# Kernel optimization log

Measured on AMD Instinct MI355X. Metric: run time of the kernel, lower is better.

Reference implementation:

```python
import jax, jax.numpy as jnp
import numpy as np

D_MODEL = 1024
D_STATE = 16
D_CONV = 4
EXPAND = 2
D_INNER = D_MODEL * EXPAND
LN_EPS = 1e-5


def setup_inputs() -> dict:
    key = jax.random.key(0)
    ks = jax.random.split(key, 12)
    s = lambda fan_in: 1.0 / np.sqrt(fan_in)
    return {
        "x": jax.random.normal(ks[0], (4, 2048, D_MODEL), dtype=jnp.float32),
        "ln_w": jnp.ones((D_MODEL,), jnp.float32),
        "ln_b": jnp.zeros((D_MODEL,), jnp.float32),
        "W_in": jax.random.uniform(ks[1], (D_MODEL, 2 * D_INNER), jnp.float32, -s(D_MODEL), s(D_MODEL)),
        "b_in": jax.random.uniform(ks[2], (2 * D_INNER,), jnp.float32, -s(D_MODEL), s(D_MODEL)),
        "conv_w": jax.random.uniform(ks[3], (D_INNER, 1, D_CONV), jnp.float32, -s(D_CONV), s(D_CONV)),
        "conv_b": jax.random.uniform(ks[4], (D_INNER,), jnp.float32, -s(D_CONV), s(D_CONV)),
        "A_log": jax.random.normal(ks[5], (D_INNER, D_STATE), jnp.float32),
        "D": jax.random.normal(ks[6], (D_INNER,), jnp.float32),
        "W_x": jax.random.uniform(ks[7], (D_INNER, 2 * D_STATE), jnp.float32, -s(D_INNER), s(D_INNER)),
        "b_x": jax.random.uniform(ks[8], (2 * D_STATE,), jnp.float32, -s(D_INNER), s(D_INNER)),
        "W_out": jax.random.uniform(ks[9], (D_INNER, D_MODEL), jnp.float32, -s(D_INNER), s(D_INNER)),
        "b_out": jax.random.uniform(ks[10], (D_MODEL,), jnp.float32, -s(D_INNER), s(D_INNER)),
    }


def _selective_scan(xc, deltaA, Bm, Cm):
    # xc: (b, s, di), deltaA: (di, n), Bm/Cm: (b, s, n)
    b, _, di = xc.shape
    n = Bm.shape[-1]
    h0 = jnp.zeros((b, di, n), xc.dtype)

    def step(h, inp):
        xt, bt, ct = inp  # (b,di), (b,n), (b,n)
        h = deltaA[None] * h + xt[:, :, None] * bt[:, None, :]
        y = jnp.einsum('bin,bn->bi', h, ct)
        return h, y

    xs = (jnp.swapaxes(xc, 0, 1), jnp.swapaxes(Bm, 0, 1), jnp.swapaxes(Cm, 0, 1))
    _, ys = jax.lax.scan(step, h0, xs)  # ys: (s, b, di)
    return jnp.swapaxes(ys, 0, 1)


def reference(x, ln_w, ln_b, W_in, b_in, conv_w, conv_b, A_log, D, W_x, b_x, W_out, b_out):
    residual = x
    mu = jnp.mean(x, -1, keepdims=True)
    var = jnp.mean((x - mu) ** 2, -1, keepdims=True)
    xn = (x - mu) * jax.lax.rsqrt(var + LN_EPS) * ln_w + ln_b
    xg = xn @ W_in + b_in
    x_main, gate = jnp.split(xg, 2, axis=-1)  # (b,s,di) each
    # causal depthwise conv1d (left pad d_conv-1 == torch pad both + slice [:s])
    xt = jnp.swapaxes(x_main, 1, 2)  # (b, di, s)
    xc = jax.lax.conv_general_dilated(
        xt, conv_w, window_strides=(1,), padding=[(D_CONV - 1, 0)],
        feature_group_count=D_INNER, dimension_numbers=('NCH', 'OIH', 'NCH'))
    xc = xc + conv_b[None, :, None]
    x_conv = jax.nn.silu(jnp.swapaxes(xc, 1, 2))  # (b,s,di)
    ssm = x_conv @ W_x + b_x
    Bm, Cm = jnp.split(ssm, 2, axis=-1)  # (b,s,n)
    deltaA = jnp.exp(-jnp.exp(A_log))  # exp(A), A = -exp(A_log)
    y = _selective_scan(x_conv, deltaA, Bm, Cm)
    y = y + x_conv * D[None, None, :]
    y = y * jax.nn.silu(gate)
    out = y @ W_out + b_out
    return out + residual
```

## Files before the change

kernel.cpp:

```cpp
#include <hip/hip_runtime.h>
#include <stdint.h>

typedef unsigned short u16;
typedef short bf16x8 __attribute__((ext_vector_type(8)));
typedef float f32x4 __attribute__((ext_vector_type(4)));

#define TOKENS 8192
#define SEQ 2048
#define DM 1024
#define DI 2048
#define NCH 32
#define CLEN 64

__device__ __forceinline__ float bf2f(u16 u) {
  union { uint32_t i; float f; } v; v.i = ((uint32_t)u) << 16; return v.f;
}
__device__ __forceinline__ u16 f2bf(float f) {
  union { float f; uint32_t i; } v; v.f = f;
  uint32_t r = v.i + 0x7FFFu + ((v.i >> 16) & 1u);
  return (u16)(r >> 16);
}

__device__ __forceinline__ void g2lds16(const void* g, void* l) {
  __builtin_amdgcn_global_load_lds(
      (const __attribute__((address_space(1))) uint32_t*)g,
      (__attribute__((address_space(3))) uint32_t*)l, 16, 0, 0);
}

__global__ __launch_bounds__(256)
void transpose_to_bf16(const float* __restrict__ src, u16* __restrict__ dst,
                       int R, int C) {
  __shared__ float tile[64][65];
  const int i = threadIdx.x;
  const int tilesC = C >> 6;
  const int br = blockIdx.x / tilesC, bc = blockIdx.x % tilesC;
  const int r0 = br << 6, c0 = bc << 6;
  const int cx = (i & 15) << 2, ry = i >> 4;
#pragma unroll
  for (int p = 0; p < 4; ++p) {
    int row = ry + p * 16;
    float4 v = *(const float4*)&src[(size_t)(r0 + row) * C + c0 + cx];
    tile[row][cx + 0] = v.x; tile[row][cx + 1] = v.y;
    tile[row][cx + 2] = v.z; tile[row][cx + 3] = v.w;
  }
  __syncthreads();
#pragma unroll
  for (int p = 0; p < 4; ++p) {
    int cr = ry + p * 16;
    ushort4 o;
    o.x = f2bf(tile[cx + 0][cr]); o.y = f2bf(tile[cx + 1][cr]);
    o.z = f2bf(tile[cx + 2][cr]); o.w = f2bf(tile[cx + 3][cr]);
    *(ushort4*)&dst[(size_t)(c0 + cr) * R + r0 + cx] = o;
  }
}

__global__ __launch_bounds__(256)
void txpose_wx(const float* __restrict__ src, u16* __restrict__ dst) {
  const int gid = blockIdx.x * 256 + threadIdx.x;
  const int k = gid >> 5, n = gid & 31;
  dst[(size_t)n * DI + k] = f2bf(src[gid]);
}

__global__ __launch_bounds__(256)
void layernorm_bf16(const float* __restrict__ x, const float* __restrict__ lw,
                    const float* __restrict__ lb, u16* __restrict__ xn) {
  const int row = blockIdx.x, tid = threadIdx.x;
  const float4 v = *(const float4*)&x[(size_t)row * DM + tid * 4];
  float s = v.x + v.y + v.z + v.w;
  float q = v.x * v.x + v.y * v.y + v.z * v.z + v.w * v.w;
#pragma unroll
  for (int m = 1; m < 64; m <<= 1) { s += __shfl_xor(s, m); q += __shfl_xor(q, m); }
  __shared__ float red[8];
  const int w = tid >> 6, lane = tid & 63;
  if (lane == 0) { red[w] = s; red[4 + w] = q; }
  __syncthreads();
  s = red[0] + red[1] + red[2] + red[3];
  q = red[4] + red[5] + red[6] + red[7];
  const float mu = s * (1.f / DM);
  const float var = q * (1.f / DM) - mu * mu;
  const float rs = rsqrtf(var + 1e-5f);
  const float4 wv = *(const float4*)&lw[tid * 4];
  const float4 bv = *(const float4*)&lb[tid * 4];
  ushort4 o;
  o.x = f2bf((v.x - mu) * rs * wv.x + bv.x);
  o.y = f2bf((v.y - mu) * rs * wv.y + bv.y);
  o.z = f2bf((v.z - mu) * rs * wv.z + bv.z);
  o.w = f2bf((v.w - mu) * rs * wv.w + bv.w);
  *(ushort4*)&xn[(size_t)row * DM + tid * 4] = o;
}

#define TILE256 (2 * 256 * 64)
__global__ __launch_bounds__(512, 2)
void gemm8(const u16* __restrict__ A, const u16* __restrict__ Bt,
           const float* __restrict__ bias, u16* __restrict__ out,
           int M, int N, int K) {
  __shared__ __align__(16) u16 lds[2 * TILE256];
  const int tid = threadIdx.x, wid = tid >> 6, lane = tid & 63;
  const int ntiles = N >> 8;
  int bid = blockIdx.x;
  {
    const int cpx = gridDim.x >> 3;
    bid = (bid & 7) * cpx + (bid >> 3);
  }
  const int tm = bid / ntiles, tn = bid % ntiles;
  const int m0 = tm << 8, n0 = tn << 8;
  const int wm = (wid >> 2) * 128, wn = (wid & 3) * 64;
  const int fr = lane & 15, fg = lane >> 4;
  const int c0 = (fg ^ (fr & 7)) << 4;
  const int NK = K >> 6;

  f32x4 acc[8][4];
#pragma unroll
  for (int mi = 0; mi < 8; ++mi)
#pragma unroll
    for (int ni = 0; ni < 4; ++ni) acc[mi][ni] = (f32x4){0.f, 0.f, 0.f, 0.f};

  auto stage_unit = [&](int T, int isB, int u) {
    const int kt = T << 6;
    const int row = u * 64 + (tid >> 3);
    const int l = (tid & 7) ^ (row & 7);
    const u16* src = (isB ? Bt + (size_t)(n0 + row) * K
                          : A + (size_t)(m0 + row) * K) + kt + l * 8;
    g2lds16(src, lds + (size_t)(T & 1) * TILE256 + isB * 16384 + u * 4096 + tid * 8);
  };

#pragma unroll
  for (int u = 0; u < 4; ++u) stage_unit(0, 1, u);
#pragma unroll
  for (int u = 0; u < 4; ++u) stage_unit(0, 0, u);
#pragma unroll
  for (int u = 0; u < 4; ++u) stage_unit(1, 1, u);
  stage_unit(1, 0, 0); stage_unit(1, 0, 2);
  asm volatile("s_waitcnt vmcnt(6)" ::: "memory");
  __builtin_amdgcn_s_barrier();
  asm volatile("" ::: "memory");

  bf16x8 bfr[2][4];
  for (int t = 0; t < NK; ++t) {
    const char* bufA = (const char*)(lds + (t & 1) * TILE256);
    const char* bufB = bufA + 32768;
#pragma unroll
    for (int q = 0; q < 4; ++q) {
      bf16x8 af[2][2];
      if (q == 0) {
#pragma unroll
        for (int ks = 0; ks < 2; ++ks) {
          const int cb = c0 ^ (ks << 6);
#pragma unroll
          for (int ni = 0; ni < 4; ++ni)
            bfr[ks][ni] = *(const bf16x8*)(bufB + (wn + ni * 16 + fr) * 128 + cb);
        }
      }
#pragma unroll
      for (int ks = 0; ks < 2; ++ks) {
        const int cb = c0 ^ (ks << 6);
#pragma unroll
        for (int r = 0; r < 2; ++r)
          af[ks][r] = *(const bf16x8*)(bufA + (wm + (2 * q + r) * 16 + fr) * 128 + cb);
      }
      if (q == 0) {
        if (t + 1 < NK) { stage_unit(t + 1, 0, 1); stage_unit(t + 1, 0, 3); }
      } else if (q == 1) {
        if (t + 2 < NK) { stage_unit(t + 2, 1, 0); stage_unit(t + 2, 1, 1); }
      } else if (q == 2) {
        if (t + 2 < NK) { stage_unit(t + 2, 1, 2); stage_unit(t + 2, 1, 3); }
      } else {
        if (t + 2 < NK) { stage_unit(t + 2, 0, 0); stage_unit(t + 2, 0, 2); }
      }
      __builtin_amdgcn_sched_barrier(0);
      __builtin_amdgcn_s_barrier();
      asm volatile("s_waitcnt lgkmcnt(0)" ::: "memory");
      __builtin_amdgcn_sched_barrier(0);
      __builtin_amdgcn_s_setprio(1);
#pragma unroll
      for (int ks = 0; ks < 2; ++ks)
#pragma unroll
        for (int r = 0; r < 2; ++r)
#pragma unroll
          for (int ni = 0; ni < 4; ++ni)
            acc[2 * q + r][ni] = __builtin_amdgcn_mfma_f32_16x16x32_bf16(
                af[ks][r], bfr[ks][ni], acc[2 * q + r][ni], 0, 0, 0);
      __builtin_amdgcn_s_setprio(0);
      if (q == 3) {
        if (t + 2 < NK) {
          asm volatile("s_waitcnt vmcnt(6)" ::: "memory");
        } else if (t + 1 < NK) {
          asm volatile("s_waitcnt vmcnt(0)" ::: "memory");
        }
      }
      __builtin_amdgcn_s_barrier();
      asm volatile("" ::: "memory");
    }
  }

#pragma unroll
  for (int mi = 0; mi < 8; ++mi)
#pragma unroll
    for (int ni = 0; ni < 4; ++ni) {
      const int col = n0 + wn + ni * 16 + fr;
      const float bcol = bias[col];
#pragma unroll
      for (int j = 0; j < 4; ++j) {
        const int row = m0 + wm + mi * 16 + fg * 4 + j;
        out[(size_t)row * N + col] = f2bf(acc[mi][ni][j] + bcol);
      }
    }
}

#define TILE_U16 ((128 + 256) * 64)
template <int EPI>
__global__ __launch_bounds__(512, 1)
void gemm3(const u16* __restrict__ A, const u16* __restrict__ Bt,
           const float* __restrict__ bias, const float* __restrict__ resid,
           void* __restrict__ out, int M, int N, int K) {
  __shared__ __align__(16) u16 lds[3 * TILE_U16];
  const int tid = threadIdx.x, wid = tid >> 6, lane = tid & 63;
  const int ntiles = N >> 8;
  int bid = blockIdx.x;
  {
    const int cpx = gridDim.x >> 3;
    bid = (bid & 7) * cpx + (bid >> 3);
  }
  const int tm = bid / ntiles, tn = bid % ntiles;
  const int m0 = tm << 7, n0 = tn << 8;
  const int wm = (wid >> 2) * 64, wn = (wid & 3) * 64;
  const int fr = lane & 15, fg = lane >> 4;
  const int c0 = (fg ^ (fr & 7)) << 4;
  const int NK = K >> 6;

  f32x4 acc[4][4];
#pragma unroll
  for (int mi = 0; mi < 4; ++mi)
#pragma unroll
    for (int ni = 0; ni < 4; ++ni) acc[mi][ni] = (f32x4){0.f, 0.f, 0.f, 0.f};

  auto stage = [&](int T) {
    const int kt = T << 6;
    u16* buf = lds + (T % 3) * TILE_U16;
#pragma unroll
    for (int i = 0; i < 2; ++i) {
      const int s = i * 512 + tid;
      const int row = s >> 3, l = (s & 7) ^ (row & 7);
      g2lds16(A + (size_t)(m0 + row) * K + kt + l * 8, buf + s * 8);
    }
    u16* bufB = buf + 128 * 64;
#pragma unroll
    for (int i = 0; i < 4; ++i) {
      const int s = i * 512 + tid;
      const int row = s >> 3, l = (s & 7) ^ (row & 7);
      g2lds16(Bt + (size_t)(n0 + row) * K + kt + l * 8, bufB + s * 8);
    }
  };

  stage(0); stage(1); stage(2);
  asm volatile("s_waitcnt vmcnt(12)" ::: "memory");
  __builtin_amdgcn_s_barrier();
  asm volatile("" ::: "memory");

  for (int T = 0; T < NK; ++T) {
    const char* bufA = (const char*)(lds + (T % 3) * TILE_U16);
    const char* bufB = bufA + 128 * 64 * 2;
    bf16x8 af[2][4], bf_[2][4];
#pragma unroll
    for (int ks = 0; ks < 2; ++ks) {
      const int cb = c0 ^ (ks << 6);
#pragma unroll
      for (int mi = 0; mi < 4; ++mi)
        af[ks][mi] = *(const bf16x8*)(bufA + (wm + mi * 16 + fr) * 128 + cb);
#pragma unroll
      for (int ni = 0; ni < 4; ++ni)
        bf_[ks][ni] = *(const bf16x8*)(bufB + (wn + ni * 16 + fr) * 128 + cb);
    }
    __builtin_amdgcn_s_setprio(1);
#pragma unroll
    for (int ks = 0; ks < 2; ++ks)
#pragma unroll
      for (int mi = 0; mi < 4; ++mi)
#pragma unroll
        for (int ni = 0; ni < 4; ++ni)
          acc[mi][ni] = __builtin_amdgcn_mfma_f32_16x16x32_bf16(
              af[ks][mi], bf_[ks][ni], acc[mi][ni], 0, 0, 0);
    __builtin_amdgcn_s_setprio(0);
    __builtin_amdgcn_s_barrier();
    asm volatile("" ::: "memory");
    if (T + 3 < NK) {
      stage(T + 3);
      asm volatile("s_waitcnt vmcnt(12)" ::: "memory");
    } else if (T + 2 < NK) {
      asm volatile("s_waitcnt vmcnt(6)" ::: "memory");
    } else if (T + 1 < NK) {
      asm volatile("s_waitcnt vmcnt(0)" ::: "memory");
    }
    __builtin_amdgcn_s_barrier();
    asm volatile("" ::: "memory");
  }

#pragma unroll
  for (int mi = 0; mi < 4; ++mi)
#pragma unroll
    for (int ni = 0; ni < 4; ++ni) {
      const int col = n0 + wn + ni * 16 + fr;
      const float bcol = bias[col];
#pragma unroll
      for (int j = 0; j < 4; ++j) {
        const int row = m0 + wm + mi * 16 + fg * 4 + j;
        float v = acc[mi][ni][j] + bcol;
        if (EPI == 1) {
          ((float*)out)[(size_t)row * N + col] = v + resid[(size_t)row * N + col];
        } else {
          ((u16*)out)[(size_t)row * N + col] = f2bf(v);
        }
      }
    }
}

__global__ __launch_bounds__(256)
void conv_silu(const u16* __restrict__ xg, const float* __restrict__ cw,
               const float* __restrict__ cb, u16* __restrict__ xconv) {
  const int t = blockIdx.x;
  const int s = t & (SEQ - 1);
  const int d = threadIdx.x * 8;
  float xv[4][8];
#pragma unroll
  for (int j = 0; j < 4; ++j) {
    const int ss = s - 3 + j;
    if (ss >= 0) {
      uint4 u = *(const uint4*)&xg[(size_t)(t - 3 + j) * (2 * DI) + d];
      const u16* pu = (const u16*)&u;
#pragma unroll
      for (int q = 0; q < 8; ++q) xv[j][q] = bf2f(pu[q]);
    } else {
#pragma unroll
      for (int q = 0; q < 8; ++q) xv[j][q] = 0.f;
    }
  }
  u16 outp[8];
#pragma unroll
  for (int q = 0; q < 8; ++q) {
    const float4 wq = *(const float4*)&cw[(d + q) * 4];
    float a = cb[d + q] + wq.x * xv[0][q] + wq.y * xv[1][q] + wq.z * xv[2][q] +
              wq.w * xv[3][q];
    outp[q] = f2bf(a / (1.f + __expf(-a)));
  }
  *(uint4*)&xconv[(size_t)t * DI + d] = *(const uint4*)outp;
}

__global__ __launch_bounds__(256)
void bc_gemm(const u16* __restrict__ xconv, const u16* __restrict__ wxT,
             float* __restrict__ BCp) {
  __shared__ __align__(16) u16 As[128 * 64];
  __shared__ __align__(16) u16 Bs[32 * 64];
  const int tid = threadIdx.x, w = tid >> 6, lane = tid & 63;
  const int mt = blockIdx.x & 63;
  const int ks_id = blockIdx.x >> 6;
  const int m0 = mt << 7;
  const int k0 = ks_id << 9;
  const int fr = lane & 15, fg = lane >> 4;
  f32x4 acc[2][2];
#pragma unroll
  for (int mf = 0; mf < 2; ++mf)
#pragma unroll
    for (int nf = 0; nf < 2; ++nf) acc[mf][nf] = (f32x4){0.f, 0.f, 0.f, 0.f};

  for (int kt = k0; kt < k0 + 512; kt += 64) {
#pragma unroll
    for (int i = 0; i < 4; ++i) {
      int ch = w * 64 + lane + i * 256;
      int row = ch >> 3, c16 = ch & 7;
      g2lds16(xconv + (size_t)(m0 + row) * DI + kt + c16 * 8,
              (u16*)As + (size_t)(w * 64 + i * 256) * 8);
    }
    {
      int row = tid >> 3, c16 = tid & 7;
      g2lds16(wxT + (size_t)row * DI + kt + c16 * 8,
              (u16*)Bs + (size_t)(w * 64) * 8);
    }
    __syncthreads();
#pragma unroll
    for (int ks = 0; ks < 2; ++ks) {
      bf16x8 af[2], bfr[2];
#pragma unroll
      for (int mf = 0; mf < 2; ++mf)
        af[mf] = *(const bf16x8*)&As[(w * 32 + mf * 16 + fr) * 64 + ks * 32 + fg * 8];
#pragma unroll
      for (int nf = 0; nf < 2; ++nf)
        bfr[nf] = *(const bf16x8*)&Bs[(nf * 16 + fr) * 64 + ks * 32 + fg * 8];
#pragma unroll
      for (int mf = 0; mf < 2; ++mf)
#pragma unroll
        for (int nf = 0; nf < 2; ++nf)
          acc[mf][nf] = __builtin_amdgcn_mfma_f32_16x16x32_bf16(
              af[mf], bfr[nf], acc[mf][nf], 0, 0, 0);
    }
    __syncthreads();
  }
#pragma unroll
  for (int mf = 0; mf < 2; ++mf)
#pragma unroll
    for (int nf = 0; nf < 2; ++nf) {
      const int col = nf * 16 + fr;
#pragma unroll
      for (int j = 0; j < 4; ++j) {
        const int row = m0 + w * 32 + mf * 16 + fg * 4 + j;
        BCp[((size_t)ks_id * TOKENS + row) * 32 + col] = acc[mf][nf][j];
      }
    }
}

__global__ __launch_bounds__(256)
void bc_reduce(const float* __restrict__ BCp, const float* __restrict__ bx,
               float* __restrict__ BC) {
  const int gid = blockIdx.x * 256 + threadIdx.x;
  const int c = gid & 31;
  const size_t t = gid >> 5;
  float s = bx[c] + BCp[t * 32 + c] + BCp[((size_t)TOKENS + t) * 32 + c] +
            BCp[((size_t)2 * TOKENS + t) * 32 + c] +
            BCp[((size_t)3 * TOKENS + t) * 32 + c];
  BC[t * 32 + c] = s;
}

__global__ __launch_bounds__(256)
void scan_passA(const u16* __restrict__ xconv, const float* __restrict__ BC,
                const float* __restrict__ A_log, float* __restrict__ F) {
  __shared__ float bcs[CLEN * 32];
  const int blk = blockIdx.x;
  const int j = blk & (NCH - 1);
  const int dg = (blk >> 5) & 7;
  const int b = blk >> 8;
  const int tid = threadIdx.x;
  const int d = dg * 256 + tid;
  const int t0 = j * CLEN;
  {
    const float4* s4 = (const float4*)(BC + (size_t)(b * SEQ + t0) * 32);
    float4* d4 = (float4*)bcs;
#pragma unroll
    for (int i = 0; i < 2; ++i) d4[tid + i * 256] = s4[tid + i * 256];
  }
  float dA[16], h[16];
#pragma unroll
  for (int n = 0; n < 16; ++n) {
    dA[n] = __expf(-__expf(A_log[d * 16 + n]));
    h[n] = 0.f;
  }
  __syncthreads();
  const u16* xcp = xconv + (size_t)(b * SEQ + t0) * DI + d;
  for (int t = 0; t < CLEN; ++t) {
    const float xc = bf2f(*xcp);
    xcp += DI;
    const float* bt = &bcs[t * 32];
#pragma unroll
    for (int n4 = 0; n4 < 4; ++n4) {
      const float4 bv = *(const float4*)&bt[n4 * 4];
      h[4 * n4 + 0] = fmaf(dA[4 * n4 + 0], h[4 * n4 + 0], xc * bv.x);
      h[4 * n4 + 1] = fmaf(dA[4 * n4 + 1], h[4 * n4 + 1], xc * bv.y);
      h[4 * n4 + 2] = fmaf(dA[4 * n4 + 2], h[4 * n4 + 2], xc * bv.z);
      h[4 * n4 + 3] = fmaf(dA[4 * n4 + 3], h[4 * n4 + 3], xc * bv.w);
    }
  }
  float* fp = F + ((size_t)((b * NCH + j) * DI) + d) * 16;
#pragma unroll
  for (int n = 0; n < 16; n += 4) {
    float4 v = {h[n], h[n + 1], h[n + 2], h[n + 3]};
    *(float4*)&fp[n] = v;
  }
}

__global__ __launch_bounds__(256)
void scan_passB(const float* __restrict__ A_log, float* __restrict__ F) {
  const int gid = blockIdx.x * 256 + threadIdx.x;
  const int n = gid & 15;
  const int d = (gid >> 4) & (DI - 1);
  const int b = gid >> 15;
  const float dAL = __expf(-(float)CLEN * __expf(A_log[d * 16 + n]));
  float carry = 0.f;
  const size_t base = ((size_t)(b * NCH) * DI + d) * 16 + n;
  const size_t stride = (size_t)DI * 16;
  for (int j = 0; j < NCH; ++j) {
    const size_t idx = base + (size_t)j * stride;
    const float f = F[idx];
    F[idx] = carry;
    carry = fmaf(dAL, carry, f);
  }
}

__global__ __launch_bounds__(256)
void scan_passC(const u16* __restrict__ xconv, const u16* __restrict__ xg,
                const float* __restrict__ BC, const float* __restrict__ A_log,
                const float* __restrict__ Dv, const float* __restrict__ F,
                u16* __restrict__ yact) {
  __shared__ float bcs[CLEN * 32];
  const int blk = blockIdx.x;
  const int j = blk & (NCH - 1);
  const int dg = (blk >> 5) & 7;
  const int b = blk >> 8;
  const int tid = threadIdx.x;
  const int d = dg * 256 + tid;
  const int t0 = j * CLEN;
  {
    const float4* s4 = (const float4*)(BC + (size_t)(b * SEQ + t0) * 32);
    float4* d4 = (float4*)bcs;
#pragma unroll
    for (int i = 0; i < 2; ++i) d4[tid + i * 256] = s4[tid + i * 256];
  }
  float dA[16], h[16];
  const float* fp = F + ((size_t)((b * NCH + j) * DI) + d) * 16;
#pragma unroll
  for (int n = 0; n < 16; n += 4) {
    float4 v = *(const float4*)&fp[n];
    h[n] = v.x; h[n + 1] = v.y; h[n + 2] = v.z; h[n + 3] = v.w;
  }
#pragma unroll
  for (int n = 0; n < 16; ++n) dA[n] = __expf(-__expf(A_log[d * 16 + n]));
  const float Dd = Dv[d];
  __syncthreads();
  const u16* xcp = xconv + (size_t)(b * SEQ + t0) * DI + d;
  const u16* gp = xg + (size_t)(b * SEQ + t0) * (2 * DI) + DI + d;
  u16* yp = yact + (size_t)(b * SEQ + t0) * DI + d;
  for (int t = 0; t < CLEN; ++t) {
    const float xc = bf2f(*xcp);
    const float g = bf2f(*gp);
    const float* bt = &bcs[t * 32];
    float y0 = 0.f, y1 = 0.f, y2 = 0.f, y3 = 0.f;
#pragma unroll
    for (int n4 = 0; n4 < 4; ++n4) {
      const float4 bv = *(const float4*)&bt[n4 * 4];
      const float4 cv = *(const float4*)&bt[16 + n4 * 4];
      const int n = 4 * n4;
      h[n]     = fmaf(dA[n],     h[n],     xc * bv.x);
      y0 = fmaf(cv.x, h[n], y0);
      h[n + 1] = fmaf(dA[n + 1], h[n + 1], xc * bv.y);
      y1 = fmaf(cv.y, h[n + 1], y1);
      h[n + 2] = fmaf(dA[n + 2], h[n + 2], xc * bv.z);
      y2 = fmaf(cv.z, h[n + 2], y2);
      h[n + 3] = fmaf(dA[n + 3], h[n + 3], xc * bv.w);
      y3 = fmaf(cv.w, h[n + 3], y3);
    }
    const float y = (y0 + y1) + (y2 + y3);
    const float ya = (y + xc * Dd) * (g / (1.f + __expf(-g)));
    *yp = f2bf(ya);
    xcp += DI; gp += 2 * DI; yp += DI;
  }
}

extern "C" void kernel_launch(void* const* d_in, const int* in_sizes, int n_in,
                              void* d_out, int out_size, void* d_ws, size_t ws_size,
                              hipStream_t stream) {
  const float* x     = (const float*)d_in[0];
  const float* ln_w  = (const float*)d_in[1];
  const float* ln_b  = (const float*)d_in[2];
  const float* W_in  = (const float*)d_in[3];
  const float* b_in  = (const float*)d_in[4];
  const float* cw    = (const float*)d_in[5];
  const float* cb    = (const float*)d_in[6];
  const float* A_log = (const float*)d_in[7];
  const float* Dv    = (const float*)d_in[8];
  const float* W_x   = (const float*)d_in[9];
  const float* b_x   = (const float*)d_in[10];
  const float* W_out = (const float*)d_in[11];
  const float* b_out = (const float*)d_in[12];

  char* ws = (char*)d_ws;
  size_t off = 0;
  auto alloc = [&](size_t bytes) {
    void* p = ws + off;
    off += (bytes + 255) & ~(size_t)255;
    return p;
  };
  u16* WinT  = (u16*)alloc((size_t)(2 * DI) * DM * 2);
  u16* WoutT = (u16*)alloc((size_t)DM * DI * 2);
  u16* xn    = (u16*)alloc((size_t)TOKENS * DM * 2);
  u16* xg    = (u16*)alloc((size_t)TOKENS * (2 * DI) * 2);
  u16* xconv = (u16*)alloc((size_t)TOKENS * DI * 2);
  float* BC  = (float*)alloc((size_t)TOKENS * 32 * 4);
  u16* yact  = (u16*)alloc((size_t)TOKENS * DI * 2);
  u16* WxT   = (u16*)alloc((size_t)32 * DI * 2);
  float* BCp = (float*)alloc((size_t)4 * TOKENS * 32 * 4);
  float* F   = (float*)xn;
  (void)ws_size; (void)in_sizes; (void)n_in; (void)out_size;

  transpose_to_bf16<<<(DM / 64) * ((2 * DI) / 64), 256, 0, stream>>>(W_in, WinT, DM, 2 * DI);
  transpose_to_bf16<<<(DI / 64) * (DM / 64), 256, 0, stream>>>(W_out, WoutT, DI, DM);
  txpose_wx<<<(DI * 32) / 256, 256, 0, stream>>>(W_x, WxT);
  layernorm_bf16<<<TOKENS, 256, 0, stream>>>(x, ln_w, ln_b, xn);
  gemm8<<<(TOKENS / 256) * ((2 * DI) / 256), 512, 0, stream>>>(
      xn, WinT, b_in, xg, TOKENS, 2 * DI, DM);
  conv_silu<<<TOKENS, 256, 0, stream>>>(xg, cw, cb, xconv);
  bc_gemm<<<256, 256, 0, stream>>>(xconv, WxT, BCp);
  bc_reduce<<<(TOKENS * 32) / 256, 256, 0, stream>>>(BCp, b_x, BC);
  scan_passA<<<4 * 8 * NCH, 256, 0, stream>>>(xconv, BC, A_log, F);
  scan_passB<<<512, 256, 0, stream>>>(A_log, F);
  scan_passC<<<4 * 8 * NCH, 256, 0, stream>>>(xconv, xg, BC, A_log, Dv, F, yact);
  gemm3<1><<<(TOKENS / 128) * (DM / 256), 512, 0, stream>>>(
      yact, WoutT, b_out, x, d_out, TOKENS, DM, DI);
}
```

Baseline: 383.2 us.

## Split-K the output projection with 256x256 tiles and a separate reduce kernel

Replaces the dedicated 128x256 output GEMM with the 256x256 gemm8 kernel run as 4-way split-K, writing bf16 partials into the now-dead xg buffer. A new out_reduce kernel sums the partials and adds the bias and residual. This aims to fill the GPU better, since the unsplit output GEMM has only 128 large tiles. It also adds unroll-2 pragmas to the scan time loops. The cost is extra partial-sum traffic, an extra launch, and bf16 rounding of the partials before the final fp32 sum.

```diff
diff --git a/kernel.cpp b/kernel.cpp
--- a/kernel.cpp
+++ b/kernel.cpp
@@ -90,6 +90,7 @@
 }
 
 #define TILE256 (2 * 256 * 64)
+template <int EPI, int KSPL>
 __global__ __launch_bounds__(512, 2)
 void gemm8(const u16* __restrict__ A, const u16* __restrict__ Bt,
            const float* __restrict__ bias, u16* __restrict__ out,
@@ -102,12 +103,17 @@
     const int cpx = gridDim.x >> 3;
     bid = (bid & 7) * cpx + (bid >> 3);
   }
-  const int tm = bid / ntiles, tn = bid % ntiles;
+  const int mnt = (M >> 8) * ntiles;
+  const int ksp = (KSPL > 1) ? (bid / mnt) : 0;
+  const int mnb = (KSPL > 1) ? (bid % mnt) : bid;
+  const int klen = K / KSPL;
+  const int kbase = ksp * klen;
+  const int tm = mnb / ntiles, tn = mnb % ntiles;
   const int m0 = tm << 8, n0 = tn << 8;
   const int wm = (wid >> 2) * 128, wn = (wid & 3) * 64;
   const int fr = lane & 15, fg = lane >> 4;
   const int c0 = (fg ^ (fr & 7)) << 4;
-  const int NK = K >> 6;
+  const int NK = klen >> 6;
 
   f32x4 acc[8][4];
 #pragma unroll
@@ -120,7 +126,7 @@
     const int row = u * 64 + (tid >> 3);
     const int l = (tid & 7) ^ (row & 7);
     const u16* src = (isB ? Bt + (size_t)(n0 + row) * K
-                          : A + (size_t)(m0 + row) * K) + kt + l * 8;
+                          : A + (size_t)(m0 + row) * K) + kbase + kt + l * 8;
     g2lds16(src, lds + (size_t)(T & 1) * TILE256 + isB * 16384 + u * 4096 + tid * 8);
   };
 
@@ -193,125 +199,41 @@
     }
   }
 
+  u16* outp = out + (size_t)ksp * M * N;
 #pragma unroll
   for (int mi = 0; mi < 8; ++mi)
 #pragma unroll
     for (int ni = 0; ni < 4; ++ni) {
       const int col = n0 + wn + ni * 16 + fr;
-      const float bcol = bias[col];
+      const float bcol = (EPI == 0) ? bias[col] : 0.f;
 #pragma unroll
       for (int j = 0; j < 4; ++j) {
         const int row = m0 + wm + mi * 16 + fg * 4 + j;
-        out[(size_t)row * N + col] = f2bf(acc[mi][ni][j] + bcol);
+        outp[(size_t)row * N + col] = f2bf(acc[mi][ni][j] + bcol);
       }
     }
 }
 
-#define TILE_U16 ((128 + 256) * 64)
-template <int EPI>
-__global__ __launch_bounds__(512, 1)
-void gemm3(const u16* __restrict__ A, const u16* __restrict__ Bt,
-           const float* __restrict__ bias, const float* __restrict__ resid,
-           void* __restrict__ out, int M, int N, int K) {
-  __shared__ __align__(16) u16 lds[3 * TILE_U16];
-  const int tid = threadIdx.x, wid = tid >> 6, lane = tid & 63;
-  const int ntiles = N >> 8;
-  int bid = blockIdx.x;
-  {
-    const int cpx = gridDim.x >> 3;
-    bid = (bid & 7) * cpx + (bid >> 3);
-  }
-  const int tm = bid / ntiles, tn = bid % ntiles;
-  const int m0 = tm << 7, n0 = tn << 8;
-  const int wm = (wid >> 2) * 64, wn = (wid & 3) * 64;
-  const int fr = lane & 15, fg = lane >> 4;
-  const int c0 = (fg ^ (fr & 7)) << 4;
-  const int NK = K >> 6;
-
-  f32x4 acc[4][4];
-#pragma unroll
-  for (int mi = 0; mi < 4; ++mi)
-#pragma unroll
-    for (int ni = 0; ni < 4; ++ni) acc[mi][ni] = (f32x4){0.f, 0.f, 0.f, 0.f};
-
-  auto stage = [&](int T) {
-    const int kt = T << 6;
-    u16* buf = lds + (T % 3) * TILE_U16;
-#pragma unroll
-    for (int i = 0; i < 2; ++i) {
-      const int s = i * 512 + tid;
-      const int row = s >> 3, l = (s & 7) ^ (row & 7);
-      g2lds16(A + (size_t)(m0 + row) * K + kt + l * 8, buf + s * 8);
-    }
-    u16* bufB = buf + 128 * 64;
-#pragma unroll
-    for (int i = 0; i < 4; ++i) {
-      const int s = i * 512 + tid;
-      const int row = s >> 3, l = (s & 7) ^ (row & 7);
-      g2lds16(Bt + (size_t)(n0 + row) * K + kt + l * 8, bufB + s * 8);
-    }
-  };
-
-  stage(0); stage(1); stage(2);
-  asm volatile("s_waitcnt vmcnt(12)" ::: "memory");
-  __builtin_amdgcn_s_barrier();
-  asm volatile("" ::: "memory");
-
-  for (int T = 0; T < NK; ++T) {
-    const char* bufA = (const char*)(lds + (T % 3) * TILE_U16);
-    const char* bufB = bufA + 128 * 64 * 2;
-    bf16x8 af[2][4], bf_[2][4];
-#pragma unroll
-    for (int ks = 0; ks < 2; ++ks) {
-      const int cb = c0 ^ (ks << 6);
-#pragma unroll
-      for (int mi = 0; mi < 4; ++mi)
-        af[ks][mi] = *(const bf16x8*)(bufA + (wm + mi * 16 + fr) * 128 + cb);
-#pragma unroll
-      for (int ni = 0; ni < 4; ++ni)
-        bf_[ks][ni] = *(const bf16x8*)(bufB + (wn + ni * 16 + fr) * 128 + cb);
-    }
-    __builtin_amdgcn_s_setprio(1);
-#pragma unroll
-    for (int ks = 0; ks < 2; ++ks)
-#pragma unroll
-      for (int mi = 0; mi < 4; ++mi)
-#pragma unroll
-        for (int ni = 0; ni < 4; ++ni)
-          acc[mi][ni] = __builtin_amdgcn_mfma_f32_16x16x32_bf16(
-              af[ks][mi], bf_[ks][ni], acc[mi][ni], 0, 0, 0);
-    __builtin_amdgcn_s_setprio(0);
-    __builtin_amdgcn_s_barrier();
-    asm volatile("" ::: "memory");
-    if (T + 3 < NK) {
-      stage(T + 3);
-      asm volatile("s_waitcnt vmcnt(12)" ::: "memory");
-    } else if (T + 2 < NK) {
-      asm volatile("s_waitcnt vmcnt(6)" ::: "memory");
-    } else if (T + 1 < NK) {
-      asm volatile("s_waitcnt vmcnt(0)" ::: "memory");
-    }
-    __builtin_amdgcn_s_barrier();
-    asm volatile("" ::: "memory");
-  }
-
-#pragma unroll
-  for (int mi = 0; mi < 4; ++mi)
-#pragma unroll
-    for (int ni = 0; ni < 4; ++ni) {
-      const int col = n0 + wn + ni * 16 + fr;
-      const float bcol = bias[col];
-#pragma unroll
-      for (int j = 0; j < 4; ++j) {
-        const int row = m0 + wm + mi * 16 + fg * 4 + j;
-        float v = acc[mi][ni][j] + bcol;
-        if (EPI == 1) {
-          ((float*)out)[(size_t)row * N + col] = v + resid[(size_t)row * N + col];
-        } else {
-          ((u16*)out)[(size_t)row * N + col] = f2bf(v);
-        }
-      }
-    }
+__global__ __launch_bounds__(256)
+void out_reduce(const u16* __restrict__ part, const float* __restrict__ x,
+                const float* __restrict__ bias, float* __restrict__ out) {
+  const int total4 = TOKENS * DM / 4;
+  for (int b4 = blockIdx.x * 256 + threadIdx.x; b4 < total4; b4 += gridDim.x * 256) {
+    const int i4 = b4 * 4;
+    const int c = i4 & (DM - 1);
+    const float4 xv = *(const float4*)&x[i4];
+    const float4 bv = *(const float4*)&bias[c];
+    float s0 = 0.f, s1 = 0.f, s2 = 0.f, s3 = 0.f;
+#pragma unroll
+    for (int sp = 0; sp < 4; ++sp) {
+      const ushort4 p = *(const ushort4*)&part[(size_t)sp * TOKENS * DM + i4];
+      s0 += bf2f(p.x); s1 += bf2f(p.y); s2 += bf2f(p.z); s3 += bf2f(p.w);
+    }
+    float4 o;
+    o.x = s0 + xv.x + bv.x; o.y = s1 + xv.y + bv.y;
+    o.z = s2 + xv.z + bv.z; o.w = s3 + xv.w + bv.w;
+    *(float4*)&out[i4] = o;
+  }
 }
 
 __global__ __launch_bounds__(256)
@@ -444,6 +366,7 @@
   }
   __syncthreads();
   const u16* xcp = xconv + (size_t)(b * SEQ + t0) * DI + d;
+#pragma unroll 2
   for (int t = 0; t < CLEN; ++t) {
     const float xc = bf2f(*xcp);
     xcp += DI;
@@ -516,6 +439,7 @@
   const u16* xcp = xconv + (size_t)(b * SEQ + t0) * DI + d;
   const u16* gp = xg + (size_t)(b * SEQ + t0) * (2 * DI) + DI + d;
   u16* yp = yact + (size_t)(b * SEQ + t0) * DI + d;
+#pragma unroll 2
   for (int t = 0; t < CLEN; ++t) {
     const float xc = bf2f(*xcp);
     const float g = bf2f(*gp);
@@ -576,13 +500,14 @@
   u16* WxT   = (u16*)alloc((size_t)32 * DI * 2);
   float* BCp = (float*)alloc((size_t)4 * TOKENS * 32 * 4);
   float* F   = (float*)xn;
+  u16* Gpart = xg;
   (void)ws_size; (void)in_sizes; (void)n_in; (void)out_size;
 
   transpose_to_bf16<<<(DM / 64) * ((2 * DI) / 64), 256, 0, stream>>>(W_in, WinT, DM, 2 * DI);
   transpose_to_bf16<<<(DI / 64) * (DM / 64), 256, 0, stream>>>(W_out, WoutT, DI, DM);
   txpose_wx<<<(DI * 32) / 256, 256, 0, stream>>>(W_x, WxT);
   layernorm_bf16<<<TOKENS, 256, 0, stream>>>(x, ln_w, ln_b, xn);
-  gemm8<<<(TOKENS / 256) * ((2 * DI) / 256), 512, 0, stream>>>(
+  gemm8<0, 1><<<(TOKENS / 256) * ((2 * DI) / 256), 512, 0, stream>>>(
       xn, WinT, b_in, xg, TOKENS, 2 * DI, DM);
   conv_silu<<<TOKENS, 256, 0, stream>>>(xg, cw, cb, xconv);
   bc_gemm<<<256, 256, 0, stream>>>(xconv, WxT, BCp);
@@ -590,6 +515,7 @@
   scan_passA<<<4 * 8 * NCH, 256, 0, stream>>>(xconv, BC, A_log, F);
   scan_passB<<<512, 256, 0, stream>>>(A_log, F);
   scan_passC<<<4 * 8 * NCH, 256, 0, stream>>>(xconv, xg, BC, A_log, Dv, F, yact);
-  gemm3<1><<<(TOKENS / 128) * (DM / 256), 512, 0, stream>>>(
-      yact, WoutT, b_out, x, d_out, TOKENS, DM, DI);
-}
+  gemm8<2, 4><<<(TOKENS / 256) * (DM / 256) * 4, 512, 0, stream>>>(
+      yact, WoutT, nullptr, Gpart, TOKENS, DM, DI);
+  out_reduce<<<2048, 256, 0, stream>>>(Gpart, x, b_out, (float*)d_out);
+}
```

After: 405.9 us. 1.06x slower.
